# Performance work log

Measured on AMD Instinct MI355X. Metric: run time of the kernel, lower is better.

Reference implementation:

```python
import jax, jax.numpy as jnp
import numpy as np

S, B, D = 2048, 2, 1024          # seq, batch, hidden
E, K = 64, 2                     # num_experts, top_k
I, SI = 512, 512                 # moe_intermediate, shared_expert_intermediate
CAP = 256                        # per-expert capacity; mean load = S*B*K/E = 128, 256 is >16 sigma -> no drops


def setup_inputs() -> dict:
    key = jax.random.key(0)
    ks = jax.random.split(key, 8)
    sc = lambda d: 1.0 / np.sqrt(d)
    return {
        "hidden_states": jax.random.normal(ks[0], (S, B, D), jnp.float32),
        "router_w": jax.random.normal(ks[1], (E, D), jnp.float32) * sc(D),          # FujiTopKRouter.weight
        "gate_up_proj": jax.random.normal(ks[2], (E, 2 * I, D), jnp.float32) * sc(D),
        "down_proj": jax.random.normal(ks[3], (E, D, I), jnp.float32) * sc(I),
        "sh_gate_w": jax.random.normal(ks[4], (SI, D), jnp.float32) * sc(D),
        "sh_up_w": jax.random.normal(ks[5], (SI, D), jnp.float32) * sc(D),
        "sh_down_w": jax.random.normal(ks[6], (D, SI), jnp.float32) * sc(SI),
        "sh_expert_gate_w": jax.random.normal(ks[7], (1, D), jnp.float32) * sc(D),
    }


def _moe(x, router_w, gate_up_proj, down_proj, sh_gate_w, sh_up_w, sh_down_w, sh_expert_gate_w):
    T = x.shape[0]
    # ---- shared expert (SwiGLU) + sigmoid gate ----
    shared = jnp.dot(jax.nn.silu(x @ sh_gate_w.T) * (x @ sh_up_w.T), sh_down_w.T)
    shared = jax.nn.sigmoid(x @ sh_expert_gate_w.T) * shared                      # [T, D]
    # ---- router: softmax (fp32) -> top-k -> normalize ----
    probs = jax.nn.softmax((x @ router_w.T).astype(jnp.float32), axis=-1)         # [T, E]
    top_w, top_i = jax.lax.top_k(probs, K)                                        # [T, K]
    top_w = top_w / (jnp.sum(top_w, axis=-1, keepdims=True) + 1e-9)
    top_w = top_w.astype(x.dtype)
    # ---- dispatch: permute (token, slot) pairs into fixed-capacity expert buffers ----
    e_f = top_i.reshape(-1)                                                       # [T*K] expert id per pair
    w_f = top_w.reshape(-1)                                                       # [T*K]
    tok = jnp.arange(T * K) // K                                                  # [T*K] source token
    oh = jax.nn.one_hot(e_f, E, dtype=jnp.int32)                                  # [T*K, E]
    pos = jnp.sum(jnp.cumsum(oh, axis=0) * oh, axis=-1) - 1                       # slot within expert
    buf = jnp.zeros((E, CAP, D), x.dtype).at[e_f, pos].set(x[tok])                # [E, C, D]
    # ---- per-expert SwiGLU as batched GEMMs ----
    h = jnp.einsum('ecd,eid->eci', buf, gate_up_proj)                             # [E, C, 2I]
    g, u = jnp.split(h, 2, axis=-1)
    y = jnp.einsum('eci,edi->ecd', jax.nn.silu(g) * u, down_proj)                 # [E, C, D]
    # ---- combine: gather back, weight, scatter-add to tokens ----
    routed = jnp.zeros_like(x).at[tok].add(y[e_f, pos] * w_f[:, None])            # [T, D]
    return shared + routed, probs


def reference(hidden_states, router_w, gate_up_proj, down_proj,
              sh_gate_w, sh_up_w, sh_down_w, sh_expert_gate_w):
    s, b, d = hidden_states.shape
    x = hidden_states.reshape(-1, d)
    out, router_logits = _moe(x, router_w, gate_up_proj, down_proj,
                              sh_gate_w, sh_up_w, sh_down_w, sh_expert_gate_w)
    return out.reshape(s, b, d), router_logits
```

## Files before the change

### kernel.cpp

```cpp
#include <hip/hip_runtime.h>
#include <hip/hip_bf16.h>
#include <stdint.h>

#define T_TOK 4096
#define DDIM  1024
#define NEXP  64
#define IDIM  512
#define SIDIM 512
#define CAP   256
#define KZ    8

typedef __attribute__((ext_vector_type(4))) float f32x4;
typedef __attribute__((ext_vector_type(8))) short bf16x8;

__device__ __forceinline__ bf16x8 cvt8(f32x4 a, f32x4 b) {
    union { __hip_bfloat162 h[4]; bf16x8 v; } u;
    u.h[0] = __float22bfloat162_rn(make_float2(a[0], a[1]));
    u.h[1] = __float22bfloat162_rn(make_float2(a[2], a[3]));
    u.h[2] = __float22bfloat162_rn(make_float2(b[0], b[1]));
    u.h[3] = __float22bfloat162_rn(make_float2(b[2], b[3]));
    return u.v;
}
__device__ __forceinline__ short f2bs(float f) {
    union { __hip_bfloat16 h; short s; } u; u.h = __float2bfloat16(f); return u.s;
}

__device__ __forceinline__ void gload16(const void* g, void* l) {
    __builtin_amdgcn_global_load_lds((const __attribute__((address_space(1))) void*)g,
                                     (__attribute__((address_space(3))) void*)l, 16, 0, 0);
}

__device__ __forceinline__ bf16x8 frag32(const char* reg0, int row, int s) {
    const char* p = reg0 + row * 128;
    int sw = row & 7;
    f32x4 lo = *(const f32x4*)(p + (((2 * s) ^ sw) << 4));
    f32x4 hi = *(const f32x4*)(p + (((2 * s + 1) ^ sw) << 4));
    return cvt8(lo, hi);
}

__global__ __launch_bounds__(256) void logits_kernel(const float* __restrict__ X,
                                                     const float* __restrict__ RW,
                                                     float* __restrict__ lpart) {
    __shared__ float sX[64 * 33];
    __shared__ float sW[64 * 33];
    int m0 = blockIdx.x * 64;
    int kz = blockIdx.y;
    int kbase = kz * (DDIM / KZ);
    int tid = threadIdx.x;
    int tg = tid >> 4;
    int eg = tid & 15;
    float acc[4][4] = {};
    for (int k0 = 0; k0 < DDIM / KZ; k0 += 32) {
        __syncthreads();
#pragma unroll
        for (int i = 0; i < 8; ++i) {
            int idx = i * 256 + tid;
            int r = idx >> 5, c = idx & 31;
            sX[r * 33 + c] = X[(size_t)(m0 + r) * DDIM + kbase + k0 + c];
            sW[r * 33 + c] = RW[(size_t)r * DDIM + kbase + k0 + c];
        }
        __syncthreads();
#pragma unroll 4
        for (int k = 0; k < 32; ++k) {
            float xv[4], wv[4];
#pragma unroll
            for (int i = 0; i < 4; ++i) xv[i] = sX[(tg * 4 + i) * 33 + k];
#pragma unroll
            for (int j = 0; j < 4; ++j) wv[j] = sW[(eg * 4 + j) * 33 + k];
#pragma unroll
            for (int i = 0; i < 4; ++i)
#pragma unroll
                for (int j = 0; j < 4; ++j) acc[i][j] += xv[i] * wv[j];
        }
    }
    float* outp = lpart + (size_t)kz * T_TOK * NEXP;
#pragma unroll
    for (int i = 0; i < 4; ++i)
#pragma unroll
        for (int j = 0; j < 4; ++j)
            outp[(size_t)(m0 + tg * 4 + i) * NEXP + eg * 4 + j] = acc[i][j];
}

__global__ __launch_bounds__(256) void topk_kernel(const float* __restrict__ lpart,
                                                   const float* __restrict__ X,
                                                   const float* __restrict__ SEG,
                                                   float* __restrict__ probs_out,
                                                   int* __restrict__ counts,
                                                   int* __restrict__ tok_slot,
                                                   float* __restrict__ w_slot,
                                                   float* __restrict__ gate_sh) {
    int lane = threadIdx.x & 63;
    int wv   = threadIdx.x >> 6;
    int t    = blockIdx.x * 4 + wv;
    size_t li = (size_t)t * NEXP + lane;
    float l = 0.f;
#pragma unroll
    for (int z = 0; z < KZ; ++z) l += lpart[(size_t)z * T_TOK * NEXP + li];
    float mx = l;
    for (int s = 32; s; s >>= 1) mx = fmaxf(mx, __shfl_xor(mx, s));
    float e = __expf(l - mx);
    float sum = e;
    for (int s = 32; s; s >>= 1) sum += __shfl_xor(sum, s);
    float prob = e / sum;
    probs_out[li] = prob;
    float v = prob; int idx = lane;
    for (int s = 32; s; s >>= 1) {
        float ov = __shfl_xor(v, s); int oi = __shfl_xor(idx, s);
        if (ov > v || (ov == v && oi < idx)) { v = ov; idx = oi; }
    }
    float v1 = v; int i1 = idx;
    v = (lane == i1) ? -1e30f : prob; idx = lane;
    for (int s = 32; s; s >>= 1) {
        float ov = __shfl_xor(v, s); int oi = __shfl_xor(idx, s);
        if (ov > v || (ov == v && oi < idx)) { v = ov; idx = oi; }
    }
    float v2 = v; int i2 = idx;
    float denom = v1 + v2 + 1e-9f;
    if (lane == 0) {
        int s1 = atomicAdd(&counts[i1], 1);
        if (s1 < CAP) { tok_slot[i1 * CAP + s1] = t; w_slot[i1 * CAP + s1] = v1 / denom; }
        int s2 = atomicAdd(&counts[i2], 1);
        if (s2 < CAP) { tok_slot[i2 * CAP + s2] = t; w_slot[i2 * CAP + s2] = v2 / denom; }
    }
    float g = 0.f;
    const float* xr = X + (size_t)t * DDIM + lane * 16;
    const float* sr = SEG + lane * 16;
#pragma unroll
    for (int j = 0; j < 4; ++j) {
        f32x4 xv = *(const f32x4*)(xr + j * 4);
        f32x4 sv = *(const f32x4*)(sr + j * 4);
#pragma unroll
        for (int q = 0; q < 4; ++q) g += xv[q] * sv[q];
    }
    for (int s = 32; s; s >>= 1) g += __shfl_xor(g, s);
    if (lane == 0) gate_sh[t] = 1.f / (1.f + __expf(-g));
}

__global__ __launch_bounds__(256, 2) void gateup_all(const float* __restrict__ X,
                                                     const float* __restrict__ GUP,
                                                     const float* __restrict__ SG,
                                                     const float* __restrict__ SU,
                                                     const int* __restrict__ counts,
                                                     const int* __restrict__ tok_slot,
                                                     short* __restrict__ act,
                                                     short* __restrict__ act_sh) {
    __shared__ char smem[2 * 32768];
    int f = blockIdx.x;
    bool expert = f < 1024;
    int e = 0, m0, n0, M;
    const float *Wg, *Wu;
    short* act_out;
    size_t out_base;
    if (expert) {
        int r = f & 7, q = (f >> 3) & 7, n = (f >> 6) & 7, y = f >> 9;
        e = q * 8 + r;
        n0 = n * 64; m0 = y * 128;
        M = counts[e]; if (M > CAP) M = CAP;
        if (m0 >= M) return;
        const float* base = GUP + (size_t)e * (2 * IDIM) * DDIM;
        Wg = base; Wu = base + (size_t)IDIM * DDIM;
        act_out = act; out_base = (size_t)e * CAP * IDIM;
    } else {
        int g = f - 1024;
        int mp = g & 31, n = g >> 5;
        n0 = n * 64; m0 = mp * 128;
        M = T_TOK; Wg = SG; Wu = SU;
        act_out = act_sh; out_base = 0;
    }
    int tid = threadIdx.x, lane = tid & 63, wv = tid >> 6;
    int wm = wv >> 1, wn = wv & 1;

    int srow8 = tid >> 3;
    int scol  = (tid & 7) ^ (srow8 & 7);
    const float* gp[8];
#pragma unroll
    for (int t = 0; t < 4; ++t) {
        int row = t * 32 + srow8;
        int grow;
        if (expert) {
            int rr = m0 + row; if (rr >= M) rr = M - 1;
            grow = tok_slot[e * CAP + rr];
        } else grow = m0 + row;
        gp[t] = X + (size_t)grow * DDIM + scol * 4;
    }
#pragma unroll
    for (int t = 0; t < 2; ++t) {
        int row = t * 32 + srow8;
        gp[4 + t] = Wg + (size_t)(n0 + row) * DDIM + scol * 4;
        gp[6 + t] = Wu + (size_t)(n0 + row) * DDIM + scol * 4;
    }

    auto issue = [&](int buf) {
        char* lb = smem + buf * 32768 + wv * 1024;
#pragma unroll
        for (int t = 0; t < 8; ++t) {
            gload16(gp[t], lb + t * 4096);
            gp[t] += 32;
        }
    };

    int fm = lane & 15, s = lane >> 4;
    f32x4 accg[4][2] = {}, accu[4][2] = {};
    auto compute = [&](int buf) {
        const char* bb = smem + buf * 32768;
        bf16x8 bg[2], bu[2];
#pragma unroll
        for (int nt = 0; nt < 2; ++nt) {
            int row = wn * 32 + nt * 16 + fm;
            bg[nt] = frag32(bb + 16384, row, s);
            bu[nt] = frag32(bb + 24576, row, s);
        }
#pragma unroll
        for (int mt = 0; mt < 4; ++mt) {
            int row = wm * 64 + mt * 16 + fm;
            bf16x8 a = frag32(bb, row, s);
#pragma unroll
            for (int nt = 0; nt < 2; ++nt) {
                accg[mt][nt] = __builtin_amdgcn_mfma_f32_16x16x32_bf16(a, bg[nt], accg[mt][nt], 0, 0, 0);
                accu[mt][nt] = __builtin_amdgcn_mfma_f32_16x16x32_bf16(a, bu[nt], accu[mt][nt], 0, 0, 0);
            }
        }
    };

    issue(0);
#pragma unroll 1
    for (int kt = 0; kt < 32; kt += 2) {
        __syncthreads();
        issue(1);
        compute(0);
        __syncthreads();
        if (kt + 2 < 32) issue(0);
        compute(1);
    }

    int frow = (lane >> 4) * 4, fcol = lane & 15;
#pragma unroll
    for (int mt = 0; mt < 4; ++mt)
#pragma unroll
        for (int r = 0; r < 4; ++r) {
            int row = m0 + wm * 64 + mt * 16 + frow + r;
            if (row < M) {
#pragma unroll
                for (int nt = 0; nt < 2; ++nt) {
                    float g = accg[mt][nt][r];
                    float u = accu[mt][nt][r];
                    float a = (g / (1.f + __expf(-g))) * u;
                    act_out[out_base + (size_t)row * IDIM + (n0 + wn * 32 + nt * 16 + fcol)] = f2bs(a);
                }
            }
        }
}

__global__ __launch_bounds__(256, 3) void down_all(const short* __restrict__ act,
                                                   const short* __restrict__ act_sh,
                                                   const float* __restrict__ DW,
                                                   const float* __restrict__ SD,
                                                   const int* __restrict__ counts,
                                                   const int* __restrict__ tok_slot,
                                                   const float* __restrict__ w_slot,
                                                   const float* __restrict__ gate_sh,
                                                   float* __restrict__ out) {
    __shared__ char smem[2 * 24576];
    const int KD = IDIM;
    int f = blockIdx.x;
    bool expert = f < 1024;
    int e = 0, m0, n0, M;
    const short* A;
    const float* W;
    if (expert) {
        int r = f & 7, q = (f >> 3) & 7, n = (f >> 6) & 7, y = f >> 9;
        e = q * 8 + r;
        n0 = n * 128; m0 = y * 128;
        M = counts[e]; if (M > CAP) M = CAP;
        if (m0 >= M) return;
        A = act + (size_t)e * CAP * IDIM;
        W = DW + (size_t)e * DDIM * IDIM;
    } else {
        int g = f - 1024;
        int mp = g & 31, n = g >> 5;
        n0 = n * 128; m0 = mp * 128;
        M = T_TOK; A = act_sh; W = SD;
    }
    int tid = threadIdx.x, lane = tid & 63, wv = tid >> 6;
    int wm = wv >> 1, wn = wv & 1;

    const short* ap[2];
#pragma unroll
    for (int t = 0; t < 2; ++t) {
        int row = t * 64 + (tid >> 2);
        int col = (tid & 3) ^ ((tid >> 2) & 3);
        ap[t] = A + (size_t)(m0 + row) * KD + col * 8;
    }
    const float* bp[4];
    {
        int srow8 = tid >> 3;
        int col = (tid & 7) ^ (srow8 & 7);
#pragma unroll
        for (int t = 0; t < 4; ++t) {
            int row = t * 32 + srow8;
            bp[t] = W + (size_t)(n0 + row) * KD + col * 4;
        }
    }

    auto issue = [&](int buf) {
        char* lb = smem + buf * 24576 + wv * 1024;
#pragma unroll
        for (int t = 0; t < 2; ++t) {
            gload16(ap[t], lb + t * 4096);
            ap[t] += 32;
        }
#pragma unroll
        for (int t = 0; t < 4; ++t) {
            gload16(bp[t], lb + 8192 + t * 4096);
            bp[t] += 32;
        }
    };

    int fm = lane & 15, s = lane >> 4;
    f32x4 acc[4][4] = {};
    auto compute = [&](int buf) {
        const char* bb = smem + buf * 24576;
        bf16x8 b[4];
#pragma unroll
        for (int nt = 0; nt < 4; ++nt) {
            int row = wn * 64 + nt * 16 + fm;
            b[nt] = frag32(bb + 8192, row, s);
        }
#pragma unroll
        for (int mt = 0; mt < 4; ++mt) {
            int row = wm * 64 + mt * 16 + fm;
            bf16x8 a = *(const bf16x8*)(bb + row * 64 + ((s ^ (row & 3)) << 4));
#pragma unroll
            for (int nt = 0; nt < 4; ++nt)
                acc[mt][nt] = __builtin_amdgcn_mfma_f32_16x16x32_bf16(a, b[nt], acc[mt][nt], 0, 0, 0);
        }
    };

    issue(0);
#pragma unroll 1
    for (int kt = 0; kt < 16; kt += 2) {
        __syncthreads();
        issue(1);
        compute(0);
        __syncthreads();
        if (kt + 2 < 16) issue(0);
        compute(1);
    }

    int frow = (lane >> 4) * 4, fcol = lane & 15;
#pragma unroll
    for (int mt = 0; mt < 4; ++mt)
#pragma unroll
        for (int r = 0; r < 4; ++r) {
            int row = m0 + wm * 64 + mt * 16 + frow + r;
            if (row >= M) continue;
            float scale; int trow;
            if (expert) { scale = w_slot[e * CAP + row]; trow = tok_slot[e * CAP + row]; }
            else        { scale = gate_sh[row];          trow = row; }
#pragma unroll
            for (int nt = 0; nt < 4; ++nt) {
                int col = n0 + wn * 64 + nt * 16 + fcol;
                atomicAdd(&out[(size_t)trow * DDIM + col], acc[mt][nt][r] * scale);
            }
        }
}

extern "C" void kernel_launch(void* const* d_in, const int* in_sizes, int n_in,
                              void* d_out, int out_size, void* d_ws, size_t ws_size,
                              hipStream_t stream) {
    const float* X   = (const float*)d_in[0];
    const float* RW  = (const float*)d_in[1];
    const float* GUP = (const float*)d_in[2];
    const float* DW  = (const float*)d_in[3];
    const float* SG  = (const float*)d_in[4];
    const float* SU  = (const float*)d_in[5];
    const float* SD  = (const float*)d_in[6];
    const float* SEG = (const float*)d_in[7];
    float* out = (float*)d_out;

    char* ws = (char*)d_ws;
    size_t off = 0;
    float* lpart    = (float*)(ws + off); off += (size_t)KZ * T_TOK * NEXP * 4;
    int*   counts   = (int*)  (ws + off); off += 1024;
    int*   tok_slot = (int*)  (ws + off); off += (size_t)NEXP * CAP * 4;
    float* w_slot   = (float*)(ws + off); off += (size_t)NEXP * CAP * 4;
    float* gate_sh  = (float*)(ws + off); off += (size_t)T_TOK * 4;
    short* act      = (short*)(ws + off); off += (size_t)NEXP * CAP * IDIM * 2;
    short* act_sh   = (short*)(ws + off); off += (size_t)T_TOK * SIDIM * 2;
    (void)ws_size; (void)in_sizes; (void)n_in; (void)out_size;

    hipMemsetAsync(counts, 0, NEXP * sizeof(int), stream);
    hipMemsetAsync(out, 0, (size_t)T_TOK * DDIM * sizeof(float), stream);
    logits_kernel<<<dim3(T_TOK / 64, KZ), 256, 0, stream>>>(X, RW, lpart);
    topk_kernel<<<T_TOK / 4, 256, 0, stream>>>(lpart, X, SEG,
                                               out + (size_t)T_TOK * DDIM,
                                               counts, tok_slot, w_slot, gate_sh);
    gateup_all<<<1280, 256, 0, stream>>>(X, GUP, SG, SU, counts, tok_slot, act, act_sh);
    down_all<<<1280, 256, 0, stream>>>(act, act_sh, DW, SD, counts, tok_slot,
                                       w_slot, gate_sh, out);
}
```

Measured before the change: 649.2 us.

## Pre-gather tokens to bf16 and use 3-stage async pipeline in expert GEMMs

Adds an xgather kernel that gathers routed tokens into per-expert bf16 buffers and converts the shared-expert input to bf16. gateup_all then loads its A operand as bf16 from a contiguous buffer instead of gathering fp32 rows. Both GEMM kernels move from a double-buffered loop with two __syncthreads per step to a single-barrier pipeline, with a triple-buffered weight stage, explicit vmcnt waits and prefetch two steps ahead. This cuts A-side global traffic and conversion work inside the GEMM and tries to hide load latency better. The cost is an extra launch plus an extra write and read of the gathered activations, and down_all's occupancy hint drops from 3 to 2 blocks per CU.

```diff
diff --git a/kernel.cpp b/kernel.cpp
--- a/kernel.cpp
+++ b/kernel.cpp
@@ -13,6 +13,11 @@
 typedef __attribute__((ext_vector_type(4))) float f32x4;
 typedef __attribute__((ext_vector_type(8))) short bf16x8;
 
+#define WAITV4 asm volatile("s_waitcnt vmcnt(4)" ::: "memory")
+#define WAITV0 asm volatile("s_waitcnt vmcnt(0)" ::: "memory")
+#define WAITL0 asm volatile("s_waitcnt lgkmcnt(0)" ::: "memory")
+#define MEMBAR asm volatile("" ::: "memory")
+
 __device__ __forceinline__ bf16x8 cvt8(f32x4 a, f32x4 b) {
     union { __hip_bfloat162 h[4]; bf16x8 v; } u;
     u.h[0] = __float22bfloat162_rn(make_float2(a[0], a[1]));
@@ -36,6 +41,9 @@
     f32x4 lo = *(const f32x4*)(p + (((2 * s) ^ sw) << 4));
     f32x4 hi = *(const f32x4*)(p + (((2 * s + 1) ^ sw) << 4));
     return cvt8(lo, hi);
+}
+__device__ __forceinline__ bf16x8 fragbf(const char* reg0, int row, int s) {
+    return *(const bf16x8*)(reg0 + row * 64 + (((s) ^ (row & 3)) << 4));
 }
 
 __global__ __launch_bounds__(256) void logits_kernel(const float* __restrict__ X,
@@ -136,21 +144,54 @@
     if (lane == 0) gate_sh[t] = 1.f / (1.f + __expf(-g));
 }
 
-__global__ __launch_bounds__(256, 2) void gateup_all(const float* __restrict__ X,
+__global__ __launch_bounds__(256) void xgather(const float* __restrict__ X,
+                                               const int* __restrict__ counts,
+                                               const int* __restrict__ tok_slot,
+                                               short* __restrict__ xg,
+                                               short* __restrict__ xsh) {
+    int b = blockIdx.x, tid = threadIdx.x;
+    if (b < 512) {
+        int r = b & 7, j = b >> 3;
+        int e = (j & 7) * 8 + r;
+        int s0 = (j >> 3) * 32;
+        int M = counts[e]; if (M > CAP) M = CAP;
+        for (int i = tid; i < 32 * 128; i += 256) {
+            int sl = s0 + (i >> 7);
+            int ch = i & 127;
+            int src = (sl < M) ? tok_slot[e * CAP + sl] : 0;
+            const float* p = X + (size_t)src * DDIM + ch * 8;
+            f32x4 lo = *(const f32x4*)p, hi = *(const f32x4*)(p + 4);
+            *(bf16x8*)(xg + ((size_t)e * CAP + sl) * DDIM + ch * 8) = cvt8(lo, hi);
+        }
+    } else {
+        int r0 = (b - 512) * 32;
+        for (int i = tid; i < 32 * 128; i += 256) {
+            int row = r0 + (i >> 7), ch = i & 127;
+            const float* p = X + (size_t)row * DDIM + ch * 8;
+            f32x4 lo = *(const f32x4*)p, hi = *(const f32x4*)(p + 4);
+            *(bf16x8*)(xsh + (size_t)row * DDIM + ch * 8) = cvt8(lo, hi);
+        }
+    }
+}
+
+__global__ __launch_bounds__(256, 2) void gateup_all(const short* __restrict__ xg,
+                                                     const short* __restrict__ xsh,
                                                      const float* __restrict__ GUP,
                                                      const float* __restrict__ SG,
                                                      const float* __restrict__ SU,
                                                      const int* __restrict__ counts,
-                                                     const int* __restrict__ tok_slot,
                                                      short* __restrict__ act,
                                                      short* __restrict__ act_sh) {
-    __shared__ char smem[2 * 32768];
+    __shared__ char sA[2 * 8192];
+    __shared__ char sB[3 * 16384];
+    const int NS = DDIM / 32;
     int f = blockIdx.x;
     bool expert = f < 1024;
     int e = 0, m0, n0, M;
     const float *Wg, *Wu;
+    const short* Abase;
     short* act_out;
-    size_t out_base;
+    size_t out_base, arow0;
     if (expert) {
         int r = f & 7, q = (f >> 3) & 7, n = (f >> 6) & 7, y = f >> 9;
         e = q * 8 + r;
@@ -159,61 +200,66 @@
         if (m0 >= M) return;
         const float* base = GUP + (size_t)e * (2 * IDIM) * DDIM;
         Wg = base; Wu = base + (size_t)IDIM * DDIM;
+        Abase = xg; arow0 = (size_t)e * CAP + m0;
         act_out = act; out_base = (size_t)e * CAP * IDIM;
     } else {
         int g = f - 1024;
         int mp = g & 31, n = g >> 5;
         n0 = n * 64; m0 = mp * 128;
         M = T_TOK; Wg = SG; Wu = SU;
+        Abase = xsh; arow0 = (size_t)m0;
         act_out = act_sh; out_base = 0;
     }
     int tid = threadIdx.x, lane = tid & 63, wv = tid >> 6;
     int wm = wv >> 1, wn = wv & 1;
 
-    int srow8 = tid >> 3;
-    int scol  = (tid & 7) ^ (srow8 & 7);
-    const float* gp[8];
-#pragma unroll
-    for (int t = 0; t < 4; ++t) {
-        int row = t * 32 + srow8;
-        int grow;
-        if (expert) {
-            int rr = m0 + row; if (rr >= M) rr = M - 1;
-            grow = tok_slot[e * CAP + rr];
-        } else grow = m0 + row;
-        gp[t] = X + (size_t)grow * DDIM + scol * 4;
-    }
+    const short* apA[2];
 #pragma unroll
     for (int t = 0; t < 2; ++t) {
-        int row = t * 32 + srow8;
-        gp[4 + t] = Wg + (size_t)(n0 + row) * DDIM + scol * 4;
-        gp[6 + t] = Wu + (size_t)(n0 + row) * DDIM + scol * 4;
-    }
-
-    auto issue = [&](int buf) {
-        char* lb = smem + buf * 32768 + wv * 1024;
-#pragma unroll
-        for (int t = 0; t < 8; ++t) {
-            gload16(gp[t], lb + t * 4096);
-            gp[t] += 32;
-        }
-    };
-
-    int fm = lane & 15, s = lane >> 4;
+        int row = (t * 4 + wv) * 16 + (lane >> 2);
+        int slot = (lane & 3) ^ ((lane >> 2) & 3);
+        apA[t] = Abase + (arow0 + row) * DDIM + slot * 8;
+    }
+    const float* bpB[4];
+#pragma unroll
+    for (int t = 0; t < 2; ++t) {
+        int row = (t * 4 + wv) * 8 + (lane >> 3);
+        int slot = (lane & 7) ^ ((lane >> 3) & 7);
+        bpB[t]     = Wg + (size_t)(n0 + row) * DDIM + slot * 4;
+        bpB[2 + t] = Wu + (size_t)(n0 + row) * DDIM + slot * 4;
+    }
+
+    auto issueA = [&](int s) {
+        char* base = sA + (s & 1) * 8192;
+#pragma unroll
+        for (int t = 0; t < 2; ++t)
+            gload16(apA[t] + s * 32, base + (t * 4 + wv) * 1024);
+    };
+    auto issueB = [&](int s) {
+        char* base = sB + (s % 3) * 16384;
+#pragma unroll
+        for (int t = 0; t < 2; ++t) {
+            gload16(bpB[t] + s * 32,     base + (t * 4 + wv) * 1024);
+            gload16(bpB[2 + t] + s * 32, base + 8192 + (t * 4 + wv) * 1024);
+        }
+    };
+
+    int fm = lane & 15, sk = lane >> 4;
     f32x4 accg[4][2] = {}, accu[4][2] = {};
-    auto compute = [&](int buf) {
-        const char* bb = smem + buf * 32768;
+    auto compute = [&](int s) {
+        const char* bbA = sA + (s & 1) * 8192;
+        const char* bbB = sB + (s % 3) * 16384;
         bf16x8 bg[2], bu[2];
 #pragma unroll
         for (int nt = 0; nt < 2; ++nt) {
             int row = wn * 32 + nt * 16 + fm;
-            bg[nt] = frag32(bb + 16384, row, s);
-            bu[nt] = frag32(bb + 24576, row, s);
+            bg[nt] = frag32(bbB, row, sk);
+            bu[nt] = frag32(bbB + 8192, row, sk);
         }
 #pragma unroll
         for (int mt = 0; mt < 4; ++mt) {
             int row = wm * 64 + mt * 16 + fm;
-            bf16x8 a = frag32(bb, row, s);
+            bf16x8 a = fragbf(bbA, row, sk);
 #pragma unroll
             for (int nt = 0; nt < 2; ++nt) {
                 accg[mt][nt] = __builtin_amdgcn_mfma_f32_16x16x32_bf16(a, bg[nt], accg[mt][nt], 0, 0, 0);
@@ -222,15 +268,16 @@
         }
     };
 
-    issue(0);
+    issueA(0); issueB(0); issueB(1);
 #pragma unroll 1
-    for (int kt = 0; kt < 32; kt += 2) {
-        __syncthreads();
-        issue(1);
-        compute(0);
-        __syncthreads();
-        if (kt + 2 < 32) issue(0);
-        compute(1);
+    for (int s = 0; s < NS; ++s) {
+        if (s < NS - 1) { WAITV4; } else { WAITV0; }
+        WAITL0;
+        __builtin_amdgcn_s_barrier();
+        MEMBAR;
+        if (s + 1 < NS) issueA(s + 1);
+        if (s + 2 < NS) issueB(s + 2);
+        compute(s);
     }
 
     int frow = (lane >> 4) * 4, fcol = lane & 15;
@@ -251,7 +298,7 @@
         }
 }
 
-__global__ __launch_bounds__(256, 3) void down_all(const short* __restrict__ act,
+__global__ __launch_bounds__(256, 2) void down_all(const short* __restrict__ act,
                                                    const short* __restrict__ act_sh,
                                                    const float* __restrict__ DW,
                                                    const float* __restrict__ SD,
@@ -260,8 +307,10 @@
                                                    const float* __restrict__ w_slot,
                                                    const float* __restrict__ gate_sh,
                                                    float* __restrict__ out) {
-    __shared__ char smem[2 * 24576];
+    __shared__ char sA[2 * 8192];
+    __shared__ char sB[3 * 16384];
     const int KD = IDIM;
+    const int NS = KD / 32;
     int f = blockIdx.x;
     bool expert = f < 1024;
     int e = 0, m0, n0, M;
@@ -284,67 +333,65 @@
     int tid = threadIdx.x, lane = tid & 63, wv = tid >> 6;
     int wm = wv >> 1, wn = wv & 1;
 
-    const short* ap[2];
+    const short* apA[2];
 #pragma unroll
     for (int t = 0; t < 2; ++t) {
-        int row = t * 64 + (tid >> 2);
-        int col = (tid & 3) ^ ((tid >> 2) & 3);
-        ap[t] = A + (size_t)(m0 + row) * KD + col * 8;
-    }
-    const float* bp[4];
-    {
-        int srow8 = tid >> 3;
-        int col = (tid & 7) ^ (srow8 & 7);
-#pragma unroll
-        for (int t = 0; t < 4; ++t) {
-            int row = t * 32 + srow8;
-            bp[t] = W + (size_t)(n0 + row) * KD + col * 4;
-        }
-    }
-
-    auto issue = [&](int buf) {
-        char* lb = smem + buf * 24576 + wv * 1024;
-#pragma unroll
-        for (int t = 0; t < 2; ++t) {
-            gload16(ap[t], lb + t * 4096);
-            ap[t] += 32;
-        }
-#pragma unroll
-        for (int t = 0; t < 4; ++t) {
-            gload16(bp[t], lb + 8192 + t * 4096);
-            bp[t] += 32;
-        }
-    };
-
-    int fm = lane & 15, s = lane >> 4;
+        int row = (t * 4 + wv) * 16 + (lane >> 2);
+        int slot = (lane & 3) ^ ((lane >> 2) & 3);
+        apA[t] = A + (size_t)(m0 + row) * KD + slot * 8;
+    }
+    const float* bpB[4];
+#pragma unroll
+    for (int t = 0; t < 4; ++t) {
+        int row = (t * 4 + wv) * 8 + (lane >> 3);
+        int slot = (lane & 7) ^ ((lane >> 3) & 7);
+        bpB[t] = W + (size_t)(n0 + row) * KD + slot * 4;
+    }
+
+    auto issueA = [&](int s) {
+        char* base = sA + (s & 1) * 8192;
+#pragma unroll
+        for (int t = 0; t < 2; ++t)
+            gload16(apA[t] + s * 32, base + (t * 4 + wv) * 1024);
+    };
+    auto issueB = [&](int s) {
+        char* base = sB + (s % 3) * 16384;
+#pragma unroll
+        for (int t = 0; t < 4; ++t)
+            gload16(bpB[t] + s * 32, base + (t * 4 + wv) * 1024);
+    };
+
+    int fm = lane & 15, sk = lane >> 4;
     f32x4 acc[4][4] = {};
-    auto compute = [&](int buf) {
-        const char* bb = smem + buf * 24576;
+    auto compute = [&](int s) {
+        const char* bbA = sA + (s & 1) * 8192;
+        const char* bbB = sB + (s % 3) * 16384;
         bf16x8 b[4];
 #pragma unroll
         for (int nt = 0; nt < 4; ++nt) {
             int row = wn * 64 + nt * 16 + fm;
-            b[nt] = frag32(bb + 8192, row, s);
+            b[nt] = frag32(bbB, row, sk);
         }
 #pragma unroll
         for (int mt = 0; mt < 4; ++mt) {
             int row = wm * 64 + mt * 16 + fm;
-            bf16x8 a = *(const bf16x8*)(bb + row * 64 + ((s ^ (row & 3)) << 4));
+            bf16x8 a = fragbf(bbA, row, sk);
 #pragma unroll
             for (int nt = 0; nt < 4; ++nt)
                 acc[mt][nt] = __builtin_amdgcn_mfma_f32_16x16x32_bf16(a, b[nt], acc[mt][nt], 0, 0, 0);
         }
     };
 
-    issue(0);
+    issueA(0); issueB(0); issueB(1);
 #pragma unroll 1
-    for (int kt = 0; kt < 16; kt += 2) {
-        __syncthreads();
-        issue(1);
-        compute(0);
-        __syncthreads();
-        if (kt + 2 < 16) issue(0);
-        compute(1);
+    for (int s = 0; s < NS; ++s) {
+        if (s < NS - 1) { WAITV4; } else { WAITV0; }
+        WAITL0;
+        __builtin_amdgcn_s_barrier();
+        MEMBAR;
+        if (s + 1 < NS) issueA(s + 1);
+        if (s + 2 < NS) issueB(s + 2);
+        compute(s);
     }
 
     int frow = (lane >> 4) * 4, fcol = lane & 15;
@@ -387,6 +434,8 @@
     float* gate_sh  = (float*)(ws + off); off += (size_t)T_TOK * 4;
     short* act      = (short*)(ws + off); off += (size_t)NEXP * CAP * IDIM * 2;
     short* act_sh   = (short*)(ws + off); off += (size_t)T_TOK * SIDIM * 2;
+    short* xg       = (short*)(ws + off); off += (size_t)NEXP * CAP * DDIM * 2;
+    short* xsh      = (short*)(ws + off); off += (size_t)T_TOK * DDIM * 2;
     (void)ws_size; (void)in_sizes; (void)n_in; (void)out_size;
 
     hipMemsetAsync(counts, 0, NEXP * sizeof(int), stream);
@@ -395,7 +444,8 @@
     topk_kernel<<<T_TOK / 4, 256, 0, stream>>>(lpart, X, SEG,
                                                out + (size_t)T_TOK * DDIM,
                                                counts, tok_slot, w_slot, gate_sh);
-    gateup_all<<<1280, 256, 0, stream>>>(X, GUP, SG, SU, counts, tok_slot, act, act_sh);
+    xgather<<<640, 256, 0, stream>>>(X, counts, tok_slot, xg, xsh);
+    gateup_all<<<1280, 256, 0, stream>>>(xg, xsh, GUP, SG, SU, counts, act, act_sh);
     down_all<<<1280, 256, 0, stream>>>(act, act_sh, DW, SD, counts, tok_slot,
                                        w_slot, gate_sh, out);
 }
```

Measured after the change: 694.5 us. 1.07x slower.
